# Optimization experiments

Measured on AMD Instinct MI355X. Metric: run time of the kernel, lower is better.

## Reference

```python
import jax, jax.numpy as jnp
import numpy as np


def setup_inputs() -> dict:
    key = jax.random.key(0)
    B, S, V = 2, 4096, 50257  # batch, seq, vocab
    x = jax.random.normal(key, (B, S, V), dtype=jnp.float32)
    return {
        "x": x,
        "k": 50,        # top-k size
        "dim": 2,       # last axis (vocab)
        "largest": 1,   # True
        "sorted": 1,    # True
    }


def reference(x, k, dim, largest, sorted):
    # aten.topk.values(x, k, dim, largest=True, sorted=True) -> (values, indices)
    # dim is the last axis here, and largest/sorted are True, which is exactly
    # jax.lax.top_k semantics (descending, sorted). For generality, move `dim`
    # to the last axis first.
    ndim = x.ndim
    d = dim % ndim
    xm = jnp.moveaxis(x, d, -1) if d != ndim - 1 else x
    vals, idx = jax.lax.top_k(xm, k)  # values sorted descending
    if d != ndim - 1:
        vals = jnp.moveaxis(vals, -1, d)
        idx = jnp.moveaxis(idx, -1, d)
    return vals, idx.astype(jnp.int64)
```

## Files before the change

kernel.cpp:

```cpp
#include <hip/hip_runtime.h>
#include <stdint.h>


#define TPB 256
#define SCAP 512
#define MCAP 2048

__device__ __forceinline__ unsigned ordf(float f) {
  unsigned s = __float_as_uint(f);
  return (s & 0x80000000u) ? ~s : (s | 0x80000000u);
}
__device__ __forceinline__ float unordf(unsigned u) {
  unsigned s = (u & 0x80000000u) ? (u ^ 0x80000000u) : ~u;
  return __uint_as_float(s);
}

__device__ __forceinline__ void bitonic_desc(float* cv, unsigned* ci, int np2, int tid) {
  for (int sz = 2; sz <= np2; sz <<= 1) {
    for (int st = sz >> 1; st > 0; st >>= 1) {
      for (int t = tid; t < (np2 >> 1); t += TPB) {
        int i = ((t & ~(st - 1)) << 1) | (t & (st - 1));
        int j = i | st;
        bool segDesc = ((i & sz) == 0);
        float va = cv[i], vb = cv[j];
        unsigned ia = ci[i], ib = ci[j];
        bool aFirst = (va > vb) || (va == vb && ia < ib);
        if (segDesc ? !aFirst : aFirst) {
          cv[i] = vb; cv[j] = va; ci[i] = ib; ci[j] = ia;
        }
      }
      __syncthreads();
    }
  }
}

__global__ __launch_bounds__(TPB) void topk_scan_kernel(
    const float* __restrict__ x, float* __restrict__ wsv,
    unsigned* __restrict__ wsi, int* __restrict__ wscnt,
    int rows, int V, int k, int cap) {
  const int row = blockIdx.x;
  const int tid = threadIdx.x;
  const float* rp = x + (size_t)row * (size_t)V;

  __shared__ float cv[SCAP];
  __shared__ unsigned ci[SCAP];
  __shared__ int s_cnt;

  unsigned mis = (unsigned)((size_t)rp & 15u);
  int head = (int)(((16u - mis) & 15u) >> 2);
  if (head > V) head = V;
  int nvec = (V - head) >> 2;
  int tail_start = head + nvec * 4;
  const float4* vp = (const float4*)(rp + head);

  unsigned lo = 0u, hi = 0xFFFFFFFFu;
  unsigned tu = ordf(2.75f);
  int cnt = 0;

  for (int attempt = 0; attempt < 48; ++attempt) {
    if (tid == 0) s_cnt = 0;
    __syncthreads();
    float thr = unordf(tu);

    for (int i = tid; i < head; i += TPB) {
      float v = rp[i];
      if (v > thr) { int p = atomicAdd(&s_cnt, 1); if (p < cap) { cv[p] = v; ci[p] = (unsigned)i; } }
    }
    for (int i = tail_start + tid; i < V; i += TPB) {
      float v = rp[i];
      if (v > thr) { int p = atomicAdd(&s_cnt, 1); if (p < cap) { cv[p] = v; ci[p] = (unsigned)i; } }
    }
    for (int j = tid; j < nvec; j += TPB) {
      float4 v = vp[j];
      float m = fmaxf(fmaxf(v.x, v.y), fmaxf(v.z, v.w));
      if (m > thr) {
        int base = head + 4 * j;
        if (v.x > thr) { int p = atomicAdd(&s_cnt, 1); if (p < cap) { cv[p] = v.x; ci[p] = (unsigned)(base + 0); } }
        if (v.y > thr) { int p = atomicAdd(&s_cnt, 1); if (p < cap) { cv[p] = v.y; ci[p] = (unsigned)(base + 1); } }
        if (v.z > thr) { int p = atomicAdd(&s_cnt, 1); if (p < cap) { cv[p] = v.z; ci[p] = (unsigned)(base + 2); } }
        if (v.w > thr) { int p = atomicAdd(&s_cnt, 1); if (p < cap) { cv[p] = v.w; ci[p] = (unsigned)(base + 3); } }
      }
    }
    __syncthreads();
    cnt = s_cnt;
    if (cnt >= k && cnt <= cap) break;
    if (hi <= lo + 1u) break;
    if (cnt > cap) lo = tu; else hi = tu;
    unsigned mid = (unsigned)(((unsigned long long)lo + (unsigned long long)hi) >> 1);
    if (mid == tu) break;
    tu = mid;
    __syncthreads();
  }
  if (cnt > cap) cnt = cap;

  if (tid == 0) wscnt[row] = cnt;
  for (int t = tid; t < cnt; t += TPB) {
    wsv[(size_t)row * cap + t] = cv[t];
    wsi[(size_t)row * cap + t] = ci[t];
  }
}

__global__ __launch_bounds__(TPB) void topk_sort_kernel(
    const float* __restrict__ wsv, const unsigned* __restrict__ wsi,
    const int* __restrict__ wscnt, float* __restrict__ out,
    int rows, int k, int cap, int out_half) {
  const int row = blockIdx.x;
  const int tid = threadIdx.x;

  __shared__ float cv[SCAP];
  __shared__ unsigned ci[SCAP];

  int cnt = wscnt[row];
  if (cnt > cap) cnt = cap;

  int np2 = 64;
  while (np2 < cnt) np2 <<= 1;

  for (int t = tid; t < cnt; t += TPB) {
    cv[t] = wsv[(size_t)row * cap + t];
    ci[t] = wsi[(size_t)row * cap + t];
  }
  for (int t = cnt + tid; t < np2; t += TPB) { cv[t] = -INFINITY; ci[t] = 0xFFFFFFFFu; }
  __syncthreads();

  bitonic_desc(cv, ci, np2, tid);

  float* out_vals = out;
  float* out_idx  = out + out_half;
  for (int t = tid; t < k; t += TPB) {
    out_vals[(size_t)row * k + t] = cv[t];
    out_idx[(size_t)row * k + t]  = (float)ci[t];
  }
}

__global__ __launch_bounds__(TPB) void topk_mono_kernel(
    const float* __restrict__ x, float* __restrict__ out,
    int rows, int V, int k, int out_half) {
  const int row = blockIdx.x;
  const int tid = threadIdx.x;
  const float* rp = x + (size_t)row * (size_t)V;

  __shared__ float cv[MCAP];
  __shared__ unsigned ci[MCAP];
  __shared__ int s_cnt;

  unsigned mis = (unsigned)((size_t)rp & 15u);
  int head = (int)(((16u - mis) & 15u) >> 2);
  if (head > V) head = V;
  int nvec = (V - head) >> 2;
  int tail_start = head + nvec * 4;
  const float4* vp = (const float4*)(rp + head);

  unsigned lo = 0u, hi = 0xFFFFFFFFu;
  unsigned tu = ordf(2.5f);
  int cnt = 0;

  for (int attempt = 0; attempt < 48; ++attempt) {
    if (tid == 0) s_cnt = 0;
    __syncthreads();
    float thr = unordf(tu);
    for (int i = tid; i < head; i += TPB) {
      float v = rp[i];
      if (v > thr) { int p = atomicAdd(&s_cnt, 1); if (p < MCAP) { cv[p] = v; ci[p] = (unsigned)i; } }
    }
    for (int i = tail_start + tid; i < V; i += TPB) {
      float v = rp[i];
      if (v > thr) { int p = atomicAdd(&s_cnt, 1); if (p < MCAP) { cv[p] = v; ci[p] = (unsigned)i; } }
    }
    for (int j = tid; j < nvec; j += TPB) {
      float4 v = vp[j];
      int base = head + 4 * j;
      if (v.x > thr) { int p = atomicAdd(&s_cnt, 1); if (p < MCAP) { cv[p] = v.x; ci[p] = (unsigned)(base + 0); } }
      if (v.y > thr) { int p = atomicAdd(&s_cnt, 1); if (p < MCAP) { cv[p] = v.y; ci[p] = (unsigned)(base + 1); } }
      if (v.z > thr) { int p = atomicAdd(&s_cnt, 1); if (p < MCAP) { cv[p] = v.z; ci[p] = (unsigned)(base + 2); } }
      if (v.w > thr) { int p = atomicAdd(&s_cnt, 1); if (p < MCAP) { cv[p] = v.w; ci[p] = (unsigned)(base + 3); } }
    }
    __syncthreads();
    cnt = s_cnt;
    if (cnt >= k && cnt <= MCAP) break;
    if (hi <= lo + 1u) break;
    if (cnt > MCAP) lo = tu; else hi = tu;
    unsigned mid = (unsigned)(((unsigned long long)lo + (unsigned long long)hi) >> 1);
    if (mid == tu) break;
    tu = mid;
    __syncthreads();
  }
  if (cnt > MCAP) cnt = MCAP;

  int np2 = 64;
  while (np2 < cnt) np2 <<= 1;
  for (int i = cnt + tid; i < np2; i += TPB) { cv[i] = -INFINITY; ci[i] = 0xFFFFFFFFu; }
  __syncthreads();

  bitonic_desc(cv, ci, np2, tid);

  float* out_vals = out;
  float* out_idx  = out + out_half;
  for (int t = tid; t < k; t += TPB) {
    out_vals[(size_t)row * k + t] = cv[t];
    out_idx[(size_t)row * k + t]  = (float)ci[t];
  }
}

extern "C" void kernel_launch(void* const* d_in, const int* in_sizes, int n_in,
                              void* d_out, int out_size, void* d_ws, size_t ws_size,
                              hipStream_t stream) {
  const float* x = (const float*)d_in[0];
  const int k = 50;
  const int out_half = out_size / 2;
  const int rows = out_half / k;
  const int V = in_sizes[0] / rows;

  int cap = 0;
  size_t cnt_off = ((size_t)rows * 4 + 255) & ~(size_t)255;
  for (int c = SCAP; c >= 128; c >>= 1) {
    size_t need = cnt_off + (size_t)rows * (size_t)c * 8;
    if (need <= ws_size) { cap = c; break; }
  }

  dim3 grid(rows), block(TPB);
  if (cap >= 128) {
    char* ws = (char*)d_ws;
    int* wscnt = (int*)ws;
    float* wsv = (float*)(ws + cnt_off);
    unsigned* wsi = (unsigned*)(ws + cnt_off + (size_t)rows * (size_t)cap * 4);
    hipLaunchKernelGGL(topk_scan_kernel, grid, block, 0, stream,
                       x, wsv, wsi, wscnt, rows, V, k, cap);
    hipLaunchKernelGGL(topk_sort_kernel, grid, block, 0, stream,
                       wsv, wsi, wscnt, (float*)d_out, rows, k, cap, out_half);
  } else {
    hipLaunchKernelGGL(topk_mono_kernel, grid, block, 0, stream,
                       x, (float*)d_out, rows, V, k, out_half);
  }
}
```

Before: 340.4 us.

## Flatten top-k threshold scan into grid-stride kernel with global per-row atomics

Replaces the one-block-per-row threshold scan with a flat grid-stride scan over the whole tensor. It runs a fixed 2048 blocks, unrolls four float4 loads per thread, and appends candidates above a fixed threshold into per-row workspace buckets using global atomics. The sort kernel now checks each row's count and, only if it falls outside [k, cap], reruns the per-row binary-search rescan itself. The aim is more uniform streaming of memory with less per-row loop overhead. The cost is an extra zeroing kernel and global atomic contention, and the workload is already close to the bandwidth limit.

```diff
diff --git a/kernel.cpp b/kernel.cpp
--- a/kernel.cpp
+++ b/kernel.cpp
@@ -5,6 +5,7 @@
 #define TPB 256
 #define SCAP 512
 #define MCAP 2048
+#define THR0 2.75f
 
 __device__ __forceinline__ unsigned ordf(float f) {
   unsigned s = __float_as_uint(f);
@@ -34,92 +35,112 @@
   }
 }
 
-__global__ __launch_bounds__(TPB) void topk_scan_kernel(
-    const float* __restrict__ x, float* __restrict__ wsv,
-    unsigned* __restrict__ wsi, int* __restrict__ wscnt,
-    int rows, int V, int k, int cap) {
+__global__ __launch_bounds__(TPB) void zero_cnt_kernel(int* __restrict__ wscnt, int rows) {
+  int i = blockIdx.x * TPB + threadIdx.x;
+  if (i < rows) wscnt[i] = 0;
+}
+
+__device__ __forceinline__ void emit_cand(float v, unsigned idx, unsigned V,
+                                          float* __restrict__ wsv,
+                                          unsigned* __restrict__ wsi,
+                                          int* __restrict__ wscnt, int cap) {
+  unsigned row = idx / V;
+  unsigned col = idx - row * V;
+  int p = atomicAdd(&wscnt[row], 1);
+  if (p < cap) {
+    wsv[(size_t)row * cap + p] = v;
+    wsi[(size_t)row * cap + p] = col;
+  }
+}
+
+__device__ __forceinline__ void proc_grp(float4 v, size_t g, float thr, unsigned V,
+                                         float* __restrict__ wsv,
+                                         unsigned* __restrict__ wsi,
+                                         int* __restrict__ wscnt, int cap) {
+  float m = fmaxf(fmaxf(v.x, v.y), fmaxf(v.z, v.w));
+  if (m > thr) {
+    unsigned e = (unsigned)(g << 2);
+    if (v.x > thr) emit_cand(v.x, e + 0u, V, wsv, wsi, wscnt, cap);
+    if (v.y > thr) emit_cand(v.y, e + 1u, V, wsv, wsi, wscnt, cap);
+    if (v.z > thr) emit_cand(v.z, e + 2u, V, wsv, wsi, wscnt, cap);
+    if (v.w > thr) emit_cand(v.w, e + 3u, V, wsv, wsi, wscnt, cap);
+  }
+}
+
+__global__ __launch_bounds__(TPB) void topk_scan_linear_kernel(
+    const float4* __restrict__ xv, size_t ngroups, int V, float thr,
+    float* __restrict__ wsv, unsigned* __restrict__ wsi,
+    int* __restrict__ wscnt, int cap) {
+  const size_t gid  = (size_t)blockIdx.x * TPB + threadIdx.x;
+  const size_t nthr = (size_t)gridDim.x * TPB;
+  const size_t step = nthr * 4;
+  const unsigned Vu = (unsigned)V;
+
+  size_t base = 0;
+  for (; base + step <= ngroups; base += step) {
+    size_t g0 = base + gid;
+    float4 v0 = xv[g0];
+    float4 v1 = xv[g0 + nthr];
+    float4 v2 = xv[g0 + 2 * nthr];
+    float4 v3 = xv[g0 + 3 * nthr];
+    proc_grp(v0, g0,            thr, Vu, wsv, wsi, wscnt, cap);
+    proc_grp(v1, g0 + nthr,     thr, Vu, wsv, wsi, wscnt, cap);
+    proc_grp(v2, g0 + 2 * nthr, thr, Vu, wsv, wsi, wscnt, cap);
+    proc_grp(v3, g0 + 3 * nthr, thr, Vu, wsv, wsi, wscnt, cap);
+  }
+  for (size_t g = base + gid; g < ngroups; g += nthr)
+    proc_grp(xv[g], g, thr, Vu, wsv, wsi, wscnt, cap);
+}
+
+__global__ __launch_bounds__(TPB) void topk_sort_kernel(
+    const float* __restrict__ x, const float* __restrict__ wsv,
+    const unsigned* __restrict__ wsi, const int* __restrict__ wscnt,
+    float* __restrict__ out, int rows, int V, int k, int cap, int out_half) {
   const int row = blockIdx.x;
   const int tid = threadIdx.x;
-  const float* rp = x + (size_t)row * (size_t)V;
 
   __shared__ float cv[SCAP];
   __shared__ unsigned ci[SCAP];
   __shared__ int s_cnt;
 
-  unsigned mis = (unsigned)((size_t)rp & 15u);
-  int head = (int)(((16u - mis) & 15u) >> 2);
-  if (head > V) head = V;
-  int nvec = (V - head) >> 2;
-  int tail_start = head + nvec * 4;
-  const float4* vp = (const float4*)(rp + head);
-
-  unsigned lo = 0u, hi = 0xFFFFFFFFu;
-  unsigned tu = ordf(2.75f);
-  int cnt = 0;
-
-  for (int attempt = 0; attempt < 48; ++attempt) {
-    if (tid == 0) s_cnt = 0;
-    __syncthreads();
-    float thr = unordf(tu);
-
-    for (int i = tid; i < head; i += TPB) {
-      float v = rp[i];
-      if (v > thr) { int p = atomicAdd(&s_cnt, 1); if (p < cap) { cv[p] = v; ci[p] = (unsigned)i; } }
-    }
-    for (int i = tail_start + tid; i < V; i += TPB) {
-      float v = rp[i];
-      if (v > thr) { int p = atomicAdd(&s_cnt, 1); if (p < cap) { cv[p] = v; ci[p] = (unsigned)i; } }
-    }
-    for (int j = tid; j < nvec; j += TPB) {
-      float4 v = vp[j];
-      float m = fmaxf(fmaxf(v.x, v.y), fmaxf(v.z, v.w));
-      if (m > thr) {
-        int base = head + 4 * j;
-        if (v.x > thr) { int p = atomicAdd(&s_cnt, 1); if (p < cap) { cv[p] = v.x; ci[p] = (unsigned)(base + 0); } }
-        if (v.y > thr) { int p = atomicAdd(&s_cnt, 1); if (p < cap) { cv[p] = v.y; ci[p] = (unsigned)(base + 1); } }
-        if (v.z > thr) { int p = atomicAdd(&s_cnt, 1); if (p < cap) { cv[p] = v.z; ci[p] = (unsigned)(base + 2); } }
-        if (v.w > thr) { int p = atomicAdd(&s_cnt, 1); if (p < cap) { cv[p] = v.w; ci[p] = (unsigned)(base + 3); } }
+  int cnt = wscnt[row];
+
+  if (cnt >= k && cnt <= cap) {
+    for (int t = tid; t < cnt; t += TPB) {
+      cv[t] = wsv[(size_t)row * cap + t];
+      ci[t] = wsi[(size_t)row * cap + t];
+    }
+  } else {
+    const float* rp = x + (size_t)row * (size_t)V;
+    unsigned lo = 0u, hi = 0xFFFFFFFFu;
+    unsigned tu = ordf(THR0);
+    cnt = 0;
+    for (int attempt = 0; attempt < 48; ++attempt) {
+      if (tid == 0) s_cnt = 0;
+      __syncthreads();
+      float thr = unordf(tu);
+      for (int i = tid; i < V; i += TPB) {
+        float v = rp[i];
+        if (v > thr) {
+          int p = atomicAdd(&s_cnt, 1);
+          if (p < SCAP) { cv[p] = v; ci[p] = (unsigned)i; }
+        }
       }
-    }
-    __syncthreads();
-    cnt = s_cnt;
-    if (cnt >= k && cnt <= cap) break;
-    if (hi <= lo + 1u) break;
-    if (cnt > cap) lo = tu; else hi = tu;
-    unsigned mid = (unsigned)(((unsigned long long)lo + (unsigned long long)hi) >> 1);
-    if (mid == tu) break;
-    tu = mid;
-    __syncthreads();
-  }
-  if (cnt > cap) cnt = cap;
-
-  if (tid == 0) wscnt[row] = cnt;
-  for (int t = tid; t < cnt; t += TPB) {
-    wsv[(size_t)row * cap + t] = cv[t];
-    wsi[(size_t)row * cap + t] = ci[t];
-  }
-}
-
-__global__ __launch_bounds__(TPB) void topk_sort_kernel(
-    const float* __restrict__ wsv, const unsigned* __restrict__ wsi,
-    const int* __restrict__ wscnt, float* __restrict__ out,
-    int rows, int k, int cap, int out_half) {
-  const int row = blockIdx.x;
-  const int tid = threadIdx.x;
-
-  __shared__ float cv[SCAP];
-  __shared__ unsigned ci[SCAP];
-
-  int cnt = wscnt[row];
-  if (cnt > cap) cnt = cap;
+      __syncthreads();
+      cnt = s_cnt;
+      if (cnt >= k && cnt <= SCAP) break;
+      if (hi <= lo + 1u) break;
+      if (cnt > SCAP) lo = tu; else hi = tu;
+      unsigned mid = (unsigned)(((unsigned long long)lo + (unsigned long long)hi) >> 1);
+      if (mid == tu) break;
+      tu = mid;
+      __syncthreads();
+    }
+    if (cnt > SCAP) cnt = SCAP;
+  }
 
   int np2 = 64;
   while (np2 < cnt) np2 <<= 1;
-
-  for (int t = tid; t < cnt; t += TPB) {
-    cv[t] = wsv[(size_t)row * cap + t];
-    ci[t] = wsi[(size_t)row * cap + t];
-  }
   for (int t = cnt + tid; t < np2; t += TPB) { cv[t] = -INFINITY; ci[t] = 0xFFFFFFFFu; }
   __syncthreads();
 
@@ -210,6 +231,7 @@
   const int out_half = out_size / 2;
   const int rows = out_half / k;
   const int V = in_sizes[0] / rows;
+  const size_t total = (size_t)in_sizes[0];
 
   int cap = 0;
   size_t cnt_off = ((size_t)rows * 4 + 255) & ~(size_t)255;
@@ -217,19 +239,26 @@
     size_t need = cnt_off + (size_t)rows * (size_t)c * 8;
     if (need <= ws_size) { cap = c; break; }
   }
-
-  dim3 grid(rows), block(TPB);
-  if (cap >= 128) {
+  bool aligned = (((size_t)x & 15u) == 0) && (total % 4 == 0);
+
+  if (cap >= 128 && aligned) {
     char* ws = (char*)d_ws;
     int* wscnt = (int*)ws;
     float* wsv = (float*)(ws + cnt_off);
     unsigned* wsi = (unsigned*)(ws + cnt_off + (size_t)rows * (size_t)cap * 4);
-    hipLaunchKernelGGL(topk_scan_kernel, grid, block, 0, stream,
-                       x, wsv, wsi, wscnt, rows, V, k, cap);
-    hipLaunchKernelGGL(topk_sort_kernel, grid, block, 0, stream,
-                       wsv, wsi, wscnt, (float*)d_out, rows, k, cap, out_half);
+
+    hipLaunchKernelGGL(zero_cnt_kernel, dim3((rows + TPB - 1) / TPB), dim3(TPB), 0, stream,
+                       wscnt, rows);
+
+    size_t ngroups = total >> 2;
+    dim3 sgrid(2048), sblock(TPB);
+    hipLaunchKernelGGL(topk_scan_linear_kernel, sgrid, sblock, 0, stream,
+                       (const float4*)x, ngroups, V, THR0, wsv, wsi, wscnt, cap);
+
+    hipLaunchKernelGGL(topk_sort_kernel, dim3(rows), dim3(TPB), 0, stream,
+                       x, wsv, wsi, wscnt, (float*)d_out, rows, V, k, cap, out_half);
   } else {
-    hipLaunchKernelGGL(topk_mono_kernel, grid, block, 0, stream,
+    hipLaunchKernelGGL(topk_mono_kernel, dim3(rows), dim3(TPB), 0, stream,
                        x, (float*)d_out, rows, V, k, out_half);
   }
 }
```

Result: slower. 516.8 us (+51.8%).
